# Kernel tuning notes

Measured on AMD Instinct MI355X. Metric: run time of the kernel, lower is better.

## Reference

```python
import jax, jax.numpy as jnp
import numpy as np

K = 1024
D = 256


def setup_inputs() -> dict:
    key = jax.random.key(0)
    k1, k2 = jax.random.split(key)
    x = jax.random.normal(k1, (32, 1024, D), dtype=jnp.float32)
    codebook = jax.random.normal(k2, (K, D), dtype=jnp.float32) / np.sqrt(D).astype(np.float32)
    return {"x": x, "codebook": codebook}


def reference(x, codebook):
    # Inference-mode forward of EMAQuantizer (EMA buffer updates are training-only side effects).
    orig_shape = x.shape
    x_flat = x.reshape(-1, D)                                   # [N, D]
    x2 = jnp.sum(x_flat * x_flat, axis=1, keepdims=True)        # [N, 1]
    e2 = jnp.sum(codebook * codebook, axis=1)[None, :]          # [1, K]
    xe = x_flat @ codebook.T                                    # [N, K]
    dist = x2 + e2 - 2.0 * xe                                   # [N, K]
    indices = jnp.argmin(dist, axis=1)                          # [N]
    x_q = codebook[indices].reshape(orig_shape)                 # gather + reshape
    # straight-through estimator
    x_q_st = x + jax.lax.stop_gradient(x_q - x)
    return x_q_st, indices.reshape(orig_shape[:-1])
```

## Files before the change

### kernel.cpp

```cpp
#include <hip/hip_runtime.h>

#define D 256

typedef __attribute__((ext_vector_type(8))) _Float16 f16x8;
typedef __attribute__((ext_vector_type(8))) short    s16x8;
typedef __attribute__((ext_vector_type(4))) float    f4_t;

__global__ __launch_bounds__(256) void conv_perm(const float* __restrict__ in,
    short* __restrict__ out, float* __restrict__ sq) {
    __shared__ float tile[16 * 264];
    const int t = threadIdx.x;
    const int p = blockIdx.x;
    const float* src = in + (size_t)p * 16 * 256;
#pragma unroll
    for (int it = 0; it < 4; ++it) {
        int idx = it * 256 + t;
        int row = idx >> 6, c4 = idx & 63;
        float4 v = *(const float4*)(src + row * 256 + c4 * 4);
        *(float4*)(tile + row * 264 + c4 * 4) = v;
    }
    __syncthreads();
    {
        int row = t >> 4, lane = t & 15;
        int b = lane >> 3, j = lane & 7;
        const float* q = tile + row * 264 + b * 128 + j;
        float r = 0.f;
        {
#pragma clang fp contract(off)
            for (int i = 0; i < 16; ++i) { float v = q[8 * i]; float s2 = v * v; r = r + s2; }
        }
        r += __shfl_xor(r, 1); r += __shfl_xor(r, 2);
        r += __shfl_xor(r, 4); r += __shfl_xor(r, 8);
        if (lane == 0) sq[p * 16 + row] = r;
    }
#pragma unroll
    for (int jj = 0; jj < 2; ++jj) {
        int sl = jj * 256 + t;
        int s = sl >> 6, chunk = (sl >> 4) & 3, rr = sl & 15;
        const float* q = tile + rr * 264 + s * 32 + chunk * 8;
        s16x8 h8;
#pragma unroll
        for (int e = 0; e < 8; ++e) {
            _Float16 hv = (_Float16)q[e];
            h8[e] = (short)__builtin_bit_cast(unsigned short, hv);
        }
        *(s16x8*)(out + (size_t)p * 4096 + (size_t)sl * 8) = h8;
    }
}

__global__ __launch_bounds__(256, 3) void vq_gemm(
    const short* __restrict__ Xh, const short* __restrict__ Eh,
    const float* __restrict__ e2, int* __restrict__ cand) {
    __shared__ short Bs[6 * 4096];
    __shared__ float e2s[256];
    const int tid = threadIdx.x;
    const int l = tid & 63;
    const int w = tid >> 6;
    const int rb = blockIdx.x & 255;
    const int q  = blockIdx.x >> 8;
    const int R0 = rb * 128;
    const int pcBase = q * 16;

#define STAGE(pp) do {                                                        \
    const short* g_ = Eh + (size_t)(pcBase + (pp)) * 4096 + w * 512 + l * 8;  \
    short* d_ = (short*)Bs + ((pp) % 6) * 4096 + w * 512;                     \
    __builtin_amdgcn_global_load_lds(                                         \
        (const __attribute__((address_space(1))) void*)g_,                    \
        (__attribute__((address_space(3))) void*)d_, 16, 0, 0);               \
    __builtin_amdgcn_global_load_lds(                                         \
        (const __attribute__((address_space(1))) void*)(g_ + 2048),           \
        (__attribute__((address_space(3))) void*)(d_ + 2048), 16, 0, 0);      \
} while (0)

    f16x8 aa[2][8];
#pragma unroll
    for (int m = 0; m < 2; ++m)
#pragma unroll
        for (int s = 0; s < 8; ++s)
            aa[m][s] = *(const f16x8*)(Xh +
                (size_t)((R0 >> 4) + w * 2 + m) * 4096 + s * 512 + l * 8);

    e2s[tid < 256 ? tid : 0] = 0.5f * e2[q * 256 + (tid < 256 ? tid : 0)];

    STAGE(0); STAGE(1); STAGE(2); STAGE(3);
    __syncthreads();

    unsigned int k1[2][4], k2[2][4];
#pragma unroll
    for (int m = 0; m < 2; ++m)
#pragma unroll
        for (int r = 0; r < 4; ++r) { k1[m][r] = 0xFFFFFFFFu; k2[m][r] = 0xFFFFFFFFu; }

#define SPBODY(S)                                                             \
    __builtin_amdgcn_s_barrier();                                             \
    asm volatile("" ::: "memory");                                            \
    _Pragma("unroll")                                                         \
    for (int hp = 0; hp < 2; ++hp) {                                          \
        const int p = 2 * (S) + hp;                                           \
        const short* bp = (const short*)Bs + (p % 6) * 4096;                  \
        f4_t acc[2][2];                                                       \
        _Pragma("unroll")                                                     \
        for (int m = 0; m < 2; ++m) {                                         \
            f4_t z = {0.f,0.f,0.f,0.f}; acc[m][0] = z; acc[m][1] = z;         \
        }                                                                     \
        {                                                                     \
            f16x8 bb[4];                                                      \
            _Pragma("unroll")                                                 \
            for (int k = 0; k < 4; ++k)                                       \
                bb[k] = *(const f16x8*)(bp + k * 512 + l * 8);                \
            _Pragma("unroll")                                                 \
            for (int k = 0; k < 4; ++k)                                       \
                _Pragma("unroll")                                             \
                for (int m = 0; m < 2; ++m)                                   \
                    acc[m][0] = __builtin_amdgcn_mfma_f32_16x16x32_f16(       \
                        aa[m][k], bb[k], acc[m][0], 0, 0, 0);                 \
        }                                                                     \
        {                                                                     \
            f16x8 bb[4];                                                      \
            _Pragma("unroll")                                                 \
            for (int k = 0; k < 4; ++k)                                       \
                bb[k] = *(const f16x8*)(bp + (k + 4) * 512 + l * 8);          \
            _Pragma("unroll")                                                 \
            for (int k = 0; k < 4; ++k)                                       \
                _Pragma("unroll")                                             \
                for (int m = 0; m < 2; ++m)                                   \
                    acc[m][1] = __builtin_amdgcn_mfma_f32_16x16x32_f16(       \
                        aa[m][k + 4], bb[k], acc[m][1], 0, 0, 0);             \
        }                                                                     \
        const unsigned int code = (unsigned int)(q * 256 + p * 16 + (l & 15));\
        const float e2b = e2s[p * 16 + (l & 15)];                             \
        _Pragma("unroll")                                                     \
        for (int m = 0; m < 2; ++m)                                           \
            _Pragma("unroll")                                                 \
            for (int r = 0; r < 4; ++r) {                                     \
                float v = e2b - (acc[m][0][r] + acc[m][1][r]);                \
                unsigned int u = __builtin_bit_cast(unsigned int, v);         \
                unsigned int f = u ^ ((unsigned int)((int)u >> 31)            \
                                     | 0x80000000u);                          \
                unsigned int key = (f & 0xFFFFFC00u) | code;                  \
                unsigned int mx = k1[m][r] > key ? k1[m][r] : key;            \
                k1[m][r] = k1[m][r] < key ? k1[m][r] : key;                   \
                k2[m][r] = k2[m][r] < mx ? k2[m][r] : mx;                     \
            }                                                                 \
    }                                                                         \
    __builtin_amdgcn_s_barrier();                                             \
    asm volatile("" ::: "memory");

#pragma unroll 1
    for (int s = 0; s < 6; ++s) {
        STAGE(2 * s + 4); STAGE(2 * s + 5);
        asm volatile("s_waitcnt vmcnt(8)" ::: "memory");
        SPBODY(s)
    }
    {
        asm volatile("s_waitcnt vmcnt(4)" ::: "memory");
        SPBODY(6)
    }
    {
        asm volatile("s_waitcnt vmcnt(0)" ::: "memory");
        SPBODY(7)
    }

    {
        int q4 = l >> 4;
#pragma unroll
        for (int m = 0; m < 2; ++m)
#pragma unroll
            for (int r = 0; r < 4; ++r) {
                unsigned int a = k1[m][r], b = k2[m][r];
#pragma unroll
                for (int msk = 1; msk < 16; msk <<= 1) {
                    unsigned int oa = __shfl_xor(a, msk);
                    unsigned int ob = __shfl_xor(b, msk);
                    unsigned int hi_ = a > oa ? a : oa;
                    a = a < oa ? a : oa;
                    b = b < ob ? b : ob;
                    b = b < hi_ ? b : hi_;
                }
                if ((l & 15) == 0) {
                    int row = R0 + w * 32 + m * 16 + q4 * 4 + r;
                    int2 o; o.x = (int)(a & 1023u); o.y = (int)(b & 1023u);
                    *(int2*)(cand + (size_t)row * 8 + q * 2) = o;
                }
            }
    }
#undef SPBODY
#undef STAGE
}

__global__ __launch_bounds__(256) void vq_decide(const float* __restrict__ x,
    const float* __restrict__ cb, const int* __restrict__ cand,
    const float* __restrict__ x2, const float* __restrict__ e2,
    float* __restrict__ outq, float* __restrict__ outi) {
    const int w = threadIdx.x >> 6, l = threadIdx.x & 63;
    const int row = blockIdx.x * 4 + w;
    const int o = l >> 3, j = l & 7;
    const int c = cand[(size_t)row * 8 + o];
    const float4* xr = (const float4*)(x + (size_t)row * D);
    const float4* er = (const float4*)(cb + (size_t)c * D);
    float xe = 0.f;
#pragma unroll
    for (int i = 0; i < 8; ++i) {
        float4 xv = xr[i * 8 + j], ev = er[i * 8 + j];
        xe = fmaf(xv.x, ev.x, xe); xe = fmaf(xv.y, ev.y, xe);
        xe = fmaf(xv.z, ev.z, xe); xe = fmaf(xv.w, ev.w, xe);
    }
    xe += __shfl_xor(xe, 1); xe += __shfl_xor(xe, 2); xe += __shfl_xor(xe, 4);
    float s0 = x2[row] + e2[c];
    float dist = s0 - 2.f * xe;
    float best = 3.4e38f; int bi = 0x7fffffff;
#pragma unroll
    for (int oq = 0; oq < 8; ++oq) {
        float dd = __shfl(dist, oq * 8);
        int   ii = __shfl(c,    oq * 8);
        if (dd < best || (dd == best && ii < bi)) { best = dd; bi = ii; }
    }
    float4 v = ((const float4*)(cb + (size_t)bi * D))[l];
    ((float4*)(outq + (size_t)row * D))[l] = v;
    if (l == 0) outi[row] = (float)bi;
}

extern "C" void kernel_launch(void* const* d_in, const int* in_sizes, int n_in,
                              void* d_out, int out_size, void* d_ws, size_t ws_size,
                              hipStream_t stream) {
    const float* x  = (const float*)d_in[0];
    const float* cb = (const float*)d_in[1];
    const int N  = in_sizes[0] / D;
    const int Kc = in_sizes[1] / D;

    float* outq = (float*)d_out;
    float* outi = outq + (size_t)N * D;

    const size_t needX = (size_t)N * D * 2;
    const size_t needS = (size_t)Kc * D * 2 + (size_t)Kc * 4
                       + (size_t)N * 4 + (size_t)N * 8 * 4;

    short* Xh; char* small;
    if (ws_size >= needX + needS) {
        Xh = (short*)d_ws;
        small = (char*)d_ws + needX;
    } else {
        Xh = (short*)d_out;
        small = (char*)d_ws;
    }
    short* Eh  = (short*)small;
    float* e2  = (float*)(Eh + (size_t)Kc * D);
    float* x2  = e2 + Kc;
    int*  cand = (int*)(x2 + N);

    conv_perm<<<N / 16, 256, 0, stream>>>(x, Xh, x2);
    conv_perm<<<Kc / 16, 256, 0, stream>>>(cb, Eh, e2);
    vq_gemm<<<(N / 128) * 4, 256, 0, stream>>>(Xh, Eh, e2, cand);
    vq_decide<<<N / 4, 256, 0, stream>>>(x, cb, cand, x2, e2, outq, outi);
}
```

Before: 65.63 us.

## Fuse conversion launches and merge GEMM with candidate rescoring in one kernel

Merges the two fp16 conversion launches into one grid. When workspace allows, it replaces the four-way-split GEMM and the separate decide kernel with a single 1024-thread block per 128 rows. That block covers all codebook columns, keeps the top-2 candidates in LDS and rescores them in fp32 before writing outputs. This drops two kernel launches and the global candidate round trip. In exchange the fused grid is only N/128 large blocks with heavy LDS use, so occupancy and parallelism are lower than before.

```diff
diff --git a/kernel.cpp b/kernel.cpp
--- a/kernel.cpp
+++ b/kernel.cpp
@@ -6,11 +6,16 @@
 typedef __attribute__((ext_vector_type(8))) short    s16x8;
 typedef __attribute__((ext_vector_type(4))) float    f4_t;
 
-__global__ __launch_bounds__(256) void conv_perm(const float* __restrict__ in,
-    short* __restrict__ out, float* __restrict__ sq) {
+__global__ __launch_bounds__(256) void conv_all(
+    const float* __restrict__ x, short* __restrict__ xh, float* __restrict__ x2,
+    const float* __restrict__ cb, short* __restrict__ eh, float* __restrict__ e2,
+    int nx) {
     __shared__ float tile[16 * 264];
     const int t = threadIdx.x;
-    const int p = blockIdx.x;
+    const int bid = blockIdx.x;
+    const float* in; short* out; float* sq; int p;
+    if (bid < nx) { in = x;  out = xh; sq = x2; p = bid; }
+    else          { in = cb; out = eh; sq = e2; p = bid - nx; }
     const float* src = in + (size_t)p * 16 * 256;
 #pragma unroll
     for (int it = 0; it < 4; ++it) {
@@ -45,6 +50,161 @@
             h8[e] = (short)__builtin_bit_cast(unsigned short, hv);
         }
         *(s16x8*)(out + (size_t)p * 4096 + (size_t)sl * 8) = h8;
+    }
+}
+
+__global__ __launch_bounds__(1024, 4) void vq_fused(
+    const short* __restrict__ Xh, const short* __restrict__ Eh,
+    const float* __restrict__ e2b_, const float* __restrict__ x2g,
+    const float* __restrict__ x, const float* __restrict__ cb,
+    float* __restrict__ outq, float* __restrict__ outi) {
+    __shared__ short Bs[2 * 6 * 4096];
+    __shared__ float e2s[1024];
+    __shared__ int   candL[128][8];
+    const int tid = threadIdx.x;
+    const int l  = tid & 63;
+    const int w  = tid >> 6;
+    const int hh = w & 1;
+    const int mg = w >> 1;
+    const int R0 = blockIdx.x * 128;
+
+#define STAGE(pp) do {                                                        \
+    const int hs_ = tid >> 9, li_ = tid & 511;                                \
+    const short* g_ = Eh + (size_t)(hs_ * 32 + (pp)) * 4096 + li_ * 8;        \
+    short* d_ = (short*)Bs + hs_ * 24576 + ((pp) % 6) * 4096 + li_ * 8;       \
+    __builtin_amdgcn_global_load_lds(                                         \
+        (const __attribute__((address_space(1))) void*)g_,                    \
+        (__attribute__((address_space(3))) void*)d_, 16, 0, 0);               \
+} while (0)
+
+    f16x8 aa[8];
+#pragma unroll
+    for (int s = 0; s < 8; ++s)
+        aa[s] = *(const f16x8*)(Xh +
+            (size_t)((R0 >> 4) + mg) * 4096 + s * 512 + l * 8);
+
+    e2s[tid] = 0.5f * e2b_[tid] + 256.0f;
+
+    STAGE(0); STAGE(1); STAGE(2); STAGE(3);
+    __syncthreads();
+
+    unsigned int k1[4], k2[4];
+#pragma unroll
+    for (int r = 0; r < 4; ++r) { k1[r] = 0xFFFFFFFFu; k2[r] = 0xFFFFFFFFu; }
+
+#define SPBODY(S)                                                             \
+    __builtin_amdgcn_s_barrier();                                             \
+    asm volatile("" ::: "memory");                                            \
+    _Pragma("unroll")                                                         \
+    for (int hp = 0; hp < 2; ++hp) {                                          \
+        const int p = 2 * (S) + hp;                                           \
+        const short* bp = (const short*)Bs + hh * 24576 + (p % 6) * 4096;     \
+        f4_t acc0 = {0.f,0.f,0.f,0.f}, acc1 = {0.f,0.f,0.f,0.f};              \
+        {                                                                     \
+            f16x8 bb[4];                                                      \
+            _Pragma("unroll")                                                 \
+            for (int k = 0; k < 4; ++k)                                       \
+                bb[k] = *(const f16x8*)(bp + k * 512 + l * 8);                \
+            _Pragma("unroll")                                                 \
+            for (int k = 0; k < 4; ++k)                                       \
+                acc0 = __builtin_amdgcn_mfma_f32_16x16x32_f16(                \
+                    aa[k], bb[k], acc0, 0, 0, 0);                             \
+        }                                                                     \
+        {                                                                     \
+            f16x8 bb[4];                                                      \
+            _Pragma("unroll")                                                 \
+            for (int k = 0; k < 4; ++k)                                       \
+                bb[k] = *(const f16x8*)(bp + (k + 4) * 512 + l * 8);          \
+            _Pragma("unroll")                                                 \
+            for (int k = 0; k < 4; ++k)                                       \
+                acc1 = __builtin_amdgcn_mfma_f32_16x16x32_f16(                \
+                    aa[k + 4], bb[k], acc1, 0, 0, 0);                         \
+        }                                                                     \
+        const unsigned int code = (unsigned int)(hh * 512 + p * 16 + (l & 15));\
+        const float e2v = e2s[hh * 512 + p * 16 + (l & 15)];                  \
+        _Pragma("unroll")                                                     \
+        for (int r = 0; r < 4; ++r) {                                         \
+            float v = e2v - (acc0[r] + acc1[r]);                              \
+            unsigned int u = __builtin_bit_cast(unsigned int, v);             \
+            unsigned int f = u ^ ((unsigned int)((int)u >> 31) | 0x80000000u);\
+            unsigned int key = (f & 0xFFFFFC00u) | code;                      \
+            unsigned int mx = k1[r] > key ? k1[r] : key;                      \
+            k1[r] = k1[r] < key ? k1[r] : key;                                \
+            k2[r] = k2[r] < mx ? k2[r] : mx;                                  \
+        }                                                                     \
+        if (p == 15 || p == 31) {                   \
+            const int q_ = hh * 2 + (p >> 4);                                 \
+            _Pragma("unroll")                                                 \
+            for (int r = 0; r < 4; ++r) {                                     \
+                unsigned int a = k1[r], b = k2[r];                            \
+                _Pragma("unroll")                                             \
+                for (int msk = 1; msk < 16; msk <<= 1) {                      \
+                    unsigned int oa = __shfl_xor(a, msk);                     \
+                    unsigned int ob = __shfl_xor(b, msk);                     \
+                    unsigned int hi_ = a > oa ? a : oa;                       \
+                    a = a < oa ? a : oa;                                      \
+                    b = b < ob ? b : ob;                                      \
+                    b = b < hi_ ? b : hi_;                                    \
+                }                                                             \
+                if ((l & 15) == 0) {                                          \
+                    int rl_ = mg * 16 + (l >> 4) * 4 + r;                     \
+                    candL[rl_][2 * q_ + 0] = (int)(a & 1023u);                \
+                    candL[rl_][2 * q_ + 1] = (int)(b & 1023u);                \
+                }                                                             \
+                k1[r] = 0xFFFFFFFFu; k2[r] = 0xFFFFFFFFu;                     \
+            }                                                                 \
+        }                                                                     \
+    }                                                                         \
+    __builtin_amdgcn_s_barrier();                                             \
+    asm volatile("" ::: "memory");
+
+#pragma unroll 1
+    for (int s = 0; s < 14; ++s) {
+        STAGE(2 * s + 4); STAGE(2 * s + 5);
+        asm volatile("s_waitcnt vmcnt(4)" ::: "memory");
+        SPBODY(s)
+    }
+    {
+        asm volatile("s_waitcnt vmcnt(2)" ::: "memory");
+        SPBODY(14)
+    }
+    {
+        asm volatile("s_waitcnt vmcnt(0)" ::: "memory");
+        SPBODY(15)
+    }
+#undef SPBODY
+#undef STAGE
+
+    __syncthreads();
+
+#pragma unroll 1
+    for (int rr = 0; rr < 8; ++rr) {
+        const int rl = w * 8 + rr;
+        const int row = R0 + rl;
+        const int o = l >> 3, j = l & 7;
+        const int c = candL[rl][o];
+        const float4* xr = (const float4*)(x + (size_t)row * D);
+        const float4* er = (const float4*)(cb + (size_t)c * D);
+        float xe = 0.f;
+#pragma unroll
+        for (int i = 0; i < 8; ++i) {
+            float4 xv = xr[i * 8 + j], ev = er[i * 8 + j];
+            xe = fmaf(xv.x, ev.x, xe); xe = fmaf(xv.y, ev.y, xe);
+            xe = fmaf(xv.z, ev.z, xe); xe = fmaf(xv.w, ev.w, xe);
+        }
+        xe += __shfl_xor(xe, 1); xe += __shfl_xor(xe, 2); xe += __shfl_xor(xe, 4);
+        float s0 = x2g[row] + e2b_[c];
+        float dist = s0 - 2.f * xe;
+        float best = 3.4e38f; int bi = 0x7fffffff;
+#pragma unroll
+        for (int oq = 0; oq < 8; ++oq) {
+            float dd = __shfl(dist, oq * 8);
+            int   ii = __shfl(c,    oq * 8);
+            if (dd < best || (dd == best && ii < bi)) { best = dd; bi = ii; }
+        }
+        float4 v = ((const float4*)(cb + (size_t)bi * D))[l];
+        ((float4*)(outq + (size_t)row * D))[l] = v;
+        if (l == 0) outi[row] = (float)bi;
     }
 }
 
@@ -160,7 +320,6 @@
         asm volatile("s_waitcnt vmcnt(0)" ::: "memory");
         SPBODY(7)
     }
-
     {
         int q4 = l >> 4;
 #pragma unroll
@@ -235,21 +394,22 @@
     const size_t needS = (size_t)Kc * D * 2 + (size_t)Kc * 4
                        + (size_t)N * 4 + (size_t)N * 8 * 4;
 
-    short* Xh; char* small;
     if (ws_size >= needX + needS) {
-        Xh = (short*)d_ws;
-        small = (char*)d_ws + needX;
+        short* Xh  = (short*)d_ws;
+        short* Eh  = Xh + (size_t)N * D;
+        float* e2  = (float*)(Eh + (size_t)Kc * D);
+        float* x2  = e2 + Kc;
+        conv_all<<<N / 16 + Kc / 16, 256, 0, stream>>>(x, Xh, x2, cb, Eh, e2, N / 16);
+        vq_fused<<<N / 128, 1024, 0, stream>>>(Xh, Eh, e2, x2, x, cb, outq, outi);
     } else {
-        Xh = (short*)d_out;
-        small = (char*)d_ws;
-    }
-    short* Eh  = (short*)small;
-    float* e2  = (float*)(Eh + (size_t)Kc * D);
-    float* x2  = e2 + Kc;
-    int*  cand = (int*)(x2 + N);
-
-    conv_perm<<<N / 16, 256, 0, stream>>>(x, Xh, x2);
-    conv_perm<<<Kc / 16, 256, 0, stream>>>(cb, Eh, e2);
-    vq_gemm<<<(N / 128) * 4, 256, 0, stream>>>(Xh, Eh, e2, cand);
-    vq_decide<<<N / 4, 256, 0, stream>>>(x, cb, cand, x2, e2, outq, outi);
+        short* Xh  = (short*)d_out;
+        char* small = (char*)d_ws;
+        short* Eh  = (short*)small;
+        float* e2  = (float*)(Eh + (size_t)Kc * D);
+        float* x2  = e2 + Kc;
+        int*  cand = (int*)(x2 + N);
+        conv_all<<<N / 16 + Kc / 16, 256, 0, stream>>>(x, Xh, x2, cb, Eh, e2, N / 16);
+        vq_gemm<<<(N / 128) * 4, 256, 0, stream>>>(Xh, Eh, e2, cand);
+        vq_decide<<<N / 4, 256, 0, stream>>>(x, cb, cand, x2, e2, outq, outi);
+    }
 }
```

Measured after the change: 64.83 us. No clear change (-1.2%).

## Merge conversion launches, shrink LDS ring, add MFMA priority and positive-bias keys

Applied to the files above, without the earlier changes.

Fuses the two fp16 conversion kernels into one launch that picks the input by block index. The GEMM kernel cuts its LDS ring buffer from six stages to four with a shallower prefetch, so four blocks can fit per CU instead of three. It also raises wave priority around the MFMA section. A +256 bias on the distance keeps it positive, so the sign-flip step in key building can be dropped. The shallower pipeline risks exposing load latency, and the bias trick assumes distances never go below -256.

```diff
diff --git a/kernel.cpp b/kernel.cpp
--- a/kernel.cpp
+++ b/kernel.cpp
@@ -6,11 +6,16 @@
 typedef __attribute__((ext_vector_type(8))) short    s16x8;
 typedef __attribute__((ext_vector_type(4))) float    f4_t;
 
-__global__ __launch_bounds__(256) void conv_perm(const float* __restrict__ in,
-    short* __restrict__ out, float* __restrict__ sq) {
+__global__ __launch_bounds__(256) void conv_all(
+    const float* __restrict__ x, short* __restrict__ xh, float* __restrict__ x2,
+    const float* __restrict__ cb, short* __restrict__ eh, float* __restrict__ e2,
+    int nx) {
     __shared__ float tile[16 * 264];
     const int t = threadIdx.x;
-    const int p = blockIdx.x;
+    const int bid = blockIdx.x;
+    const float* in; short* out; float* sq; int p;
+    if (bid < nx) { in = x;  out = xh; sq = x2; p = bid; }
+    else          { in = cb; out = eh; sq = e2; p = bid - nx; }
     const float* src = in + (size_t)p * 16 * 256;
 #pragma unroll
     for (int it = 0; it < 4; ++it) {
@@ -48,10 +53,10 @@
     }
 }
 
-__global__ __launch_bounds__(256, 3) void vq_gemm(
+__global__ __launch_bounds__(256, 4) void vq_gemm(
     const short* __restrict__ Xh, const short* __restrict__ Eh,
     const float* __restrict__ e2, int* __restrict__ cand) {
-    __shared__ short Bs[6 * 4096];
+    __shared__ short Bs[4 * 4096];
     __shared__ float e2s[256];
     const int tid = threadIdx.x;
     const int l = tid & 63;
@@ -63,7 +68,7 @@
 
 #define STAGE(pp) do {                                                        \
     const short* g_ = Eh + (size_t)(pcBase + (pp)) * 4096 + w * 512 + l * 8;  \
-    short* d_ = (short*)Bs + ((pp) % 6) * 4096 + w * 512;                     \
+    short* d_ = (short*)Bs + ((pp) & 3) * 4096 + w * 512;                     \
     __builtin_amdgcn_global_load_lds(                                         \
         (const __attribute__((address_space(1))) void*)g_,                    \
         (__attribute__((address_space(3))) void*)d_, 16, 0, 0);               \
@@ -80,9 +85,9 @@
             aa[m][s] = *(const f16x8*)(Xh +
                 (size_t)((R0 >> 4) + w * 2 + m) * 4096 + s * 512 + l * 8);
 
-    e2s[tid < 256 ? tid : 0] = 0.5f * e2[q * 256 + (tid < 256 ? tid : 0)];
-
-    STAGE(0); STAGE(1); STAGE(2); STAGE(3);
+    e2s[tid] = 0.5f * e2[q * 256 + tid] + 256.0f;
+
+    STAGE(0); STAGE(1);
     __syncthreads();
 
     unsigned int k1[2][4], k2[2][4];
@@ -97,12 +102,13 @@
     _Pragma("unroll")                                                         \
     for (int hp = 0; hp < 2; ++hp) {                                          \
         const int p = 2 * (S) + hp;                                           \
-        const short* bp = (const short*)Bs + (p % 6) * 4096;                  \
+        const short* bp = (const short*)Bs + (p & 3) * 4096;                  \
         f4_t acc[2][2];                                                       \
         _Pragma("unroll")                                                     \
         for (int m = 0; m < 2; ++m) {                                         \
             f4_t z = {0.f,0.f,0.f,0.f}; acc[m][0] = z; acc[m][1] = z;         \
         }                                                                     \
+        __builtin_amdgcn_s_setprio(1);                                        \
         {                                                                     \
             f16x8 bb[4];                                                      \
             _Pragma("unroll")                                                 \
@@ -127,6 +133,7 @@
                     acc[m][1] = __builtin_amdgcn_mfma_f32_16x16x32_f16(       \
                         aa[m][k + 4], bb[k], acc[m][1], 0, 0, 0);             \
         }                                                                     \
+        __builtin_amdgcn_s_setprio(0);                                        \
         const unsigned int code = (unsigned int)(q * 256 + p * 16 + (l & 15));\
         const float e2b = e2s[p * 16 + (l & 15)];                             \
         _Pragma("unroll")                                                     \
@@ -135,9 +142,7 @@
             for (int r = 0; r < 4; ++r) {                                     \
                 float v = e2b - (acc[m][0][r] + acc[m][1][r]);                \
                 unsigned int u = __builtin_bit_cast(unsigned int, v);         \
-                unsigned int f = u ^ ((unsigned int)((int)u >> 31)            \
-                                     | 0x80000000u);                          \
-                unsigned int key = (f & 0xFFFFFC00u) | code;                  \
+                unsigned int key = (u & 0xFFFFFC00u) | code;     \
                 unsigned int mx = k1[m][r] > key ? k1[m][r] : key;            \
                 k1[m][r] = k1[m][r] < key ? k1[m][r] : key;                   \
                 k2[m][r] = k2[m][r] < mx ? k2[m][r] : mx;                     \
@@ -147,14 +152,10 @@
     asm volatile("" ::: "memory");
 
 #pragma unroll 1
-    for (int s = 0; s < 6; ++s) {
-        STAGE(2 * s + 4); STAGE(2 * s + 5);
-        asm volatile("s_waitcnt vmcnt(8)" ::: "memory");
+    for (int s = 0; s < 7; ++s) {
+        STAGE(2 * s + 2); STAGE(2 * s + 3);
+        asm volatile("s_waitcnt vmcnt(4)" ::: "memory");
         SPBODY(s)
-    }
-    {
-        asm volatile("s_waitcnt vmcnt(4)" ::: "memory");
-        SPBODY(6)
     }
     {
         asm volatile("s_waitcnt vmcnt(0)" ::: "memory");
@@ -248,8 +249,7 @@
     float* x2  = e2 + Kc;
     int*  cand = (int*)(x2 + N);
 
-    conv_perm<<<N / 16, 256, 0, stream>>>(x, Xh, x2);
-    conv_perm<<<Kc / 16, 256, 0, stream>>>(cb, Eh, e2);
+    conv_all<<<N / 16 + Kc / 16, 256, 0, stream>>>(x, Xh, x2, cb, Eh, e2, N / 16);
     vq_gemm<<<(N / 128) * 4, 256, 0, stream>>>(Xh, Eh, e2, cand);
     vq_decide<<<N / 4, 256, 0, stream>>>(x, cb, cand, x2, e2, outq, outi);
 }
```

Result: faster. 60.53 us (-7.8%).
